# Kernel tuning notes

Measured on AMD Instinct MI355X. Metric: run time of the kernel, lower is better.

## Reference

```python
import jax, jax.numpy as jnp
import numpy as np

WIN = 7
K1, K2 = 0.01, 0.03


def _box_filter(x, w):
    """Valid-padding uniform box filter. x: (B, D, H, W); w: (1, 1, k, k)."""
    B, D, H, Wd = x.shape
    k = w.shape[-1]
    y = jax.lax.conv_general_dilated(
        x.reshape(B * D, 1, H, Wd), w, window_strides=(1, 1), padding='VALID',
        dimension_numbers=('NCHW', 'OIHW', 'NCHW'))
    return y.reshape(B, D, H - k + 1, Wd - k + 1)


def setup_inputs() -> dict:
    key = jax.random.key(0)
    kx, ky = jax.random.split(key)
    X = jax.random.uniform(kx, (4, 64, 256, 256), dtype=jnp.float32)
    Y = jax.random.uniform(ky, (4, 64, 256, 256), dtype=jnp.float32)
    w = jnp.ones((1, 1, WIN, WIN), dtype=jnp.float32) / (WIN * WIN)  # buffer self.w
    return {"X": X, "Y": Y, "w": w}


def reference(X, Y, w):
    data_range = 1.0
    C1 = (K1 * data_range) ** 2
    C2 = (K2 * data_range) ** 2
    NP = WIN * WIN
    cov_norm = NP / (NP - 1)

    ux = _box_filter(X, w)
    uy = _box_filter(Y, w)
    uxx = _box_filter(X * X, w)
    uyy = _box_filter(Y * Y, w)
    uxy = _box_filter(X * Y, w)

    vx = cov_norm * (uxx - ux * ux)
    vy = cov_norm * (uyy - uy * uy)
    vxy = cov_norm * (uxy - ux * uy)

    A1 = 2.0 * ux * uy + C1
    A2 = 2.0 * vxy + C2
    B1 = ux * ux + uy * uy + C1
    B2 = vx + vy + C2
    S = (A1 * A2) / (B1 * B2)  # (B, D, H', W')

    # Faithful to torch: ssim_per_slice[:, i] = S_i.mean() (mean over batch AND spatial),
    # then 1 - mean over depth, returned per batch element.
    slice_means = S.mean(axis=(0, 2, 3))  # (D,)
    loss = 1.0 - slice_means.mean()
    return jnp.full((X.shape[0],), loss, dtype=X.dtype)
```

## Files before the change

### kernel.cpp

```cpp
#include <hip/hip_runtime.h>

#define H 256
#define W 256
#define OWID 250
#define BAND 10
#define NBANDS 25
#define NW 3200
#define WPB 4
#define NBLOCKS (NW / WPB)
#define RIN 16
#define ROWB 1024


__device__ __forceinline__ float4 f4zero() { return make_float4(0.f, 0.f, 0.f, 0.f); }

#define CC1 1e-4f
#define CC2 9e-4f
#define KAA (1.f / 2401.f)
#define K2A (2.f / 2401.f)
#define KT1 (1.f / 24.f)
#define KT2 (-1.f / 1176.f)
#define KT3 (1.f / 48.f)
#define KT4 (-1.f / 2352.f)

struct M4 { float4 sx, sy, sxy, spp; };

__device__ __forceinline__ float4 ld16(const char* b, int off) {
    return *(const float4*)(b + off);
}

__device__ __forceinline__ void slide(M4& m, const float4 xn, const float4 yn,
                                      const float4 xo, const float4 yo) {
    m.sx.x += xn.x - xo.x; m.sx.y += xn.y - xo.y;
    m.sx.z += xn.z - xo.z; m.sx.w += xn.w - xo.w;
    m.sy.x += yn.x - yo.x; m.sy.y += yn.y - yo.y;
    m.sy.z += yn.z - yo.z; m.sy.w += yn.w - yo.w;
    m.sxy.x = fmaf(xn.x, yn.x, fmaf(-xo.x, yo.x, m.sxy.x));
    m.sxy.y = fmaf(xn.y, yn.y, fmaf(-xo.y, yo.y, m.sxy.y));
    m.sxy.z = fmaf(xn.z, yn.z, fmaf(-xo.z, yo.z, m.sxy.z));
    m.sxy.w = fmaf(xn.w, yn.w, fmaf(-xo.w, yo.w, m.sxy.w));
    m.spp.x = fmaf(xn.x, xn.x, fmaf(yn.x, yn.x, fmaf(-xo.x, xo.x, fmaf(-yo.x, yo.x, m.spp.x))));
    m.spp.y = fmaf(xn.y, xn.y, fmaf(yn.y, yn.y, fmaf(-xo.y, xo.y, fmaf(-yo.y, yo.y, m.spp.y))));
    m.spp.z = fmaf(xn.z, xn.z, fmaf(yn.z, yn.z, fmaf(-xo.z, xo.z, fmaf(-yo.z, yo.z, m.spp.z))));
    m.spp.w = fmaf(xn.w, xn.w, fmaf(yn.w, yn.w, fmaf(-xo.w, xo.w, fmaf(-yo.w, yo.w, m.spp.w))));
}

__device__ __forceinline__ void hwin4(const float4 S, float w[4]) {
    const float p1 = S.x;
    const float p2 = p1 + S.y;
    const float p3 = p2 + S.z;
    const float E  = p3 + S.w;
    const float n3 = __shfl_down(p3, 1);
    const float nE = __shfl_down(E, 1);
    const float f1 = __shfl_down(p1, 2);
    const float f2 = __shfl_down(p2, 2);
    w[0] = E + n3;
    w[1] = (E - p1) + nE;
    w[2] = (E - p2) + nE + f1;
    w[3] = (E - p3) + nE + f2;
}

__device__ __forceinline__ void outrow(const M4& m, const float m01,
                                       const float m23, float& lsum) {
    float wx[4], wy[4], wpp[4], wxy[4];
    hwin4(m.sx,  wx);
    hwin4(m.sy,  wy);
    hwin4(m.spp, wpp);
    hwin4(m.sxy, wxy);
    #pragma unroll
    for (int s = 0; s < 4; ++s) {
        const float P  = wx[s] * wy[s];
        const float Qs = fmaf(wy[s], wy[s], wx[s] * wx[s]);
        const float A1 = fmaf(K2A, P, CC1);
        const float B1 = fmaf(KAA, Qs, CC1);
        const float A2 = fmaf(KT1, wxy[s], fmaf(KT2, P, CC2));
        const float B2 = fmaf(KT3, wpp[s], fmaf(KT4, Qs, CC2));
        const float S  = (A1 * A2) * __builtin_amdgcn_rcpf(B1 * B2);
        lsum = fmaf(S, (s < 2) ? m01 : m23, lsum);
    }
}

template<int R>
__device__ __forceinline__ void step(
    const char* XA, const char* YA, const char* XB, const char* YB,
    const int lo, M4& a, M4& b,
    float4& exA, float4& eyA, float4& exB, float4& eyB,
    const float m01, const float m23, float& lsum)
{
    {
        const float4 xn = exA, yn = eyA;
        if constexpr (R + 1 < RIN) {
            exA = ld16(XA, lo + (R + 1) * ROWB);
            eyA = ld16(YA, lo + (R + 1) * ROWB);
        }
        float4 xo = f4zero(), yo = f4zero();
        if constexpr (R >= 7) {
            xo = ld16(XA, lo + (R - 7) * ROWB);
            yo = ld16(YA, lo + (R - 7) * ROWB);
        }
        slide(a, xn, yn, xo, yo);
        if constexpr (R >= 6) outrow(a, m01, m23, lsum);
    }
    {
        const float4 xn = exB, yn = eyB;
        if constexpr (R + 1 < RIN) {
            exB = ld16(XB, lo + (R + 1) * ROWB);
            eyB = ld16(YB, lo + (R + 1) * ROWB);
        }
        float4 xo = f4zero(), yo = f4zero();
        if constexpr (R >= 7) {
            xo = ld16(XB, lo + (R - 7) * ROWB);
            yo = ld16(YB, lo + (R - 7) * ROWB);
        }
        slide(b, xn, yn, xo, yo);
        if constexpr (R >= 6) outrow(b, m01, m23, lsum);
    }
    if constexpr (R + 1 < RIN)
        step<R + 1>(XA, YA, XB, YB, lo, a, b, exA, eyA, exB, eyB, m01, m23, lsum);
}

__global__ __launch_bounds__(256) void ssim_band_kernel(
    const float* __restrict__ X, const float* __restrict__ Y,
    float* __restrict__ partial)
{
    const int lane = threadIdx.x & 63;
    const int wid  = blockIdx.x * WPB + (threadIdx.x >> 6);
    const int imgA = wid / NBANDS;
    const int band = wid % NBANDS;
    const int r0 = band * BAND;

    const size_t baseA = ((size_t)imgA * H + r0) * ROWB;
    const size_t dB    = (size_t)128 * H * ROWB;
    const char* XA = (const char*)X + baseA;
    const char* YA = (const char*)Y + baseA;
    const char* XB = XA + dB;
    const char* YB = YA + dB;
    const int lo = lane * 16;

    M4 a, b;
    a.sx = f4zero(); a.sy = f4zero(); a.sxy = f4zero(); a.spp = f4zero();
    b.sx = f4zero(); b.sy = f4zero(); b.sxy = f4zero(); b.spp = f4zero();

    float4 exA = ld16(XA, lo), eyA = ld16(YA, lo);
    float4 exB = ld16(XB, lo), eyB = ld16(YB, lo);

    const float m01 = (lane <= 62) ? 1.0f : 0.0f;
    const float m23 = (lane <= 61) ? 1.0f : 0.0f;

    float lsum = 0.0f;
    step<0>(XA, YA, XB, YB, lo, a, b, exA, eyA, exB, eyB, m01, m23, lsum);

    #pragma unroll
    for (int off = 32; off > 0; off >>= 1)
        lsum += __shfl_down(lsum, off, 64);
    if (lane == 0) partial[wid] = lsum;
}

__global__ __launch_bounds__(256) void ssim_reduce_kernel(
    const float* __restrict__ partial, float* __restrict__ out)
{
    const int tid = threadIdx.x;
    double acc = 0.0;
    for (int i = tid; i < NW; i += 256)
        acc += (double)partial[i];
    #pragma unroll
    for (int off = 32; off > 0; off >>= 1)
        acc += __shfl_down(acc, off, 64);
    __shared__ double wsumd[4];
    if ((tid & 63) == 0) wsumd[tid >> 6] = acc;
    __syncthreads();
    if (tid == 0) {
        double total = wsumd[0] + wsumd[1] + wsumd[2] + wsumd[3];
        float loss = (float)(1.0 - total / 16000000.0);
        out[0] = loss; out[1] = loss; out[2] = loss; out[3] = loss;
    }
}

extern "C" void kernel_launch(void* const* d_in, const int* in_sizes, int n_in,
                              void* d_out, int out_size, void* d_ws, size_t ws_size,
                              hipStream_t stream) {
    const float* X = (const float*)d_in[0];
    const float* Y = (const float*)d_in[1];
    float* out = (float*)d_out;
    float* partial = (float*)d_ws;

    hipLaunchKernelGGL(ssim_band_kernel, dim3(NBLOCKS), dim3(256), 0, stream,
                       X, Y, partial);
    hipLaunchKernelGGL(ssim_reduce_kernel, dim3(1), dim3(256), 0, stream,
                       partial, out);
}
```

Before: 162.6 us.

## Stage band rows through LDS with async global_load_lds, one image per wave

Replaces direct register loads with global_load_lds (direct global-to-LDS DMA) into a triple-buffered ring for incoming rows and a double-buffered ring for the rows leaving the window, synchronised by explicit vmcnt waits. Each wave now handles one image band instead of two, which doubles the number of waves and partials. The intent is to overlap memory latency with compute and lower register pressure. In exchange it adds LDS traffic, relies on hand-tuned waitcnt counts being correct, and halves the work per wave.

```diff
diff --git a/kernel.cpp b/kernel.cpp
--- a/kernel.cpp
+++ b/kernel.cpp
@@ -2,14 +2,15 @@
 
 #define H 256
 #define W 256
+#define W4 (W / 4)
 #define OWID 250
 #define BAND 10
 #define NBANDS 25
-#define NW 3200
+#define NBLK 6400
+#define RIN 16
 #define WPB 4
-#define NBLOCKS (NW / WPB)
-#define RIN 16
-#define ROWB 1024
+#define NBLOCKS (NBLK / WPB)
+#define SLOTF 512
 
 
 __device__ __forceinline__ float4 f4zero() { return make_float4(0.f, 0.f, 0.f, 0.f); }
@@ -23,11 +24,26 @@
 #define KT3 (1.f / 48.f)
 #define KT4 (-1.f / 2352.f)
 
+__device__ __forceinline__ void stage(const float4* g, float* l) {
+    __builtin_amdgcn_global_load_lds(
+        (const __attribute__((address_space(1))) unsigned int*)g,
+        (__attribute__((address_space(3))) unsigned int*)l,
+        16, 0, 0);
+}
+
+template<int N> __device__ __forceinline__ void wait_vm() {
+    if constexpr (N >= 6)      asm volatile("s_waitcnt vmcnt(6)" ::: "memory");
+    else if constexpr (N == 4) asm volatile("s_waitcnt vmcnt(4)" ::: "memory");
+    else if constexpr (N == 2) asm volatile("s_waitcnt vmcnt(2)" ::: "memory");
+    else                       asm volatile("s_waitcnt vmcnt(0)" ::: "memory");
+    __builtin_amdgcn_sched_barrier(0);
+}
+
+template<int R> constexpr int nwait() {
+    return (R <= 5) ? 4 : (R <= 13) ? 6 : (R == 14) ? 4 : 0;
+}
+
 struct M4 { float4 sx, sy, sxy, spp; };
-
-__device__ __forceinline__ float4 ld16(const char* b, int off) {
-    return *(const float4*)(b + off);
-}
 
 __device__ __forceinline__ void slide(M4& m, const float4 xn, const float4 yn,
                                       const float4 xo, const float4 yo) {
@@ -81,74 +97,68 @@
 }
 
 template<int R>
-__device__ __forceinline__ void step(
-    const char* XA, const char* YA, const char* XB, const char* YB,
-    const int lo, M4& a, M4& b,
-    float4& exA, float4& eyA, float4& exB, float4& eyB,
-    const float m01, const float m23, float& lsum)
+__device__ __forceinline__ void step(const float4* Xp, const float4* Yp,
+                                     float* exl, float* lvl, const int lo4,
+                                     M4& m, const float m01, const float m23,
+                                     float& lsum)
 {
-    {
-        const float4 xn = exA, yn = eyA;
-        if constexpr (R + 1 < RIN) {
-            exA = ld16(XA, lo + (R + 1) * ROWB);
-            eyA = ld16(YA, lo + (R + 1) * ROWB);
-        }
-        float4 xo = f4zero(), yo = f4zero();
-        if constexpr (R >= 7) {
-            xo = ld16(XA, lo + (R - 7) * ROWB);
-            yo = ld16(YA, lo + (R - 7) * ROWB);
-        }
-        slide(a, xn, yn, xo, yo);
-        if constexpr (R >= 6) outrow(a, m01, m23, lsum);
-    }
-    {
-        const float4 xn = exB, yn = eyB;
-        if constexpr (R + 1 < RIN) {
-            exB = ld16(XB, lo + (R + 1) * ROWB);
-            eyB = ld16(YB, lo + (R + 1) * ROWB);
-        }
-        float4 xo = f4zero(), yo = f4zero();
-        if constexpr (R >= 7) {
-            xo = ld16(XB, lo + (R - 7) * ROWB);
-            yo = ld16(YB, lo + (R - 7) * ROWB);
-        }
-        slide(b, xn, yn, xo, yo);
-        if constexpr (R >= 6) outrow(b, m01, m23, lsum);
-    }
+    if constexpr (R >= 6 && R <= 14) {
+        stage(Xp + (R - 6) * W4, lvl + ((R - 6) % 2) * SLOTF);
+        stage(Yp + (R - 6) * W4, lvl + ((R - 6) % 2) * SLOTF + 256);
+    }
+    if constexpr (R + 2 < RIN) {
+        stage(Xp + (R + 2) * W4, exl + ((R + 2) % 3) * SLOTF);
+        stage(Yp + (R + 2) * W4, exl + ((R + 2) % 3) * SLOTF + 256);
+    }
+    wait_vm<nwait<R>()>();
+
+    const float4 xn = *(const float4*)(exl + (R % 3) * SLOTF + lo4);
+    const float4 yn = *(const float4*)(exl + (R % 3) * SLOTF + 256 + lo4);
+    float4 xo = f4zero(), yo = f4zero();
+    if constexpr (R >= 7) {
+        xo = *(const float4*)(lvl + ((R - 7) % 2) * SLOTF + lo4);
+        yo = *(const float4*)(lvl + ((R - 7) % 2) * SLOTF + 256 + lo4);
+    }
+
+    slide(m, xn, yn, xo, yo);
+    if constexpr (R >= 6) outrow(m, m01, m23, lsum);
+
     if constexpr (R + 1 < RIN)
-        step<R + 1>(XA, YA, XB, YB, lo, a, b, exA, eyA, exB, eyB, m01, m23, lsum);
+        step<R + 1>(Xp, Yp, exl, lvl, lo4, m, m01, m23, lsum);
 }
 
 __global__ __launch_bounds__(256) void ssim_band_kernel(
     const float* __restrict__ X, const float* __restrict__ Y,
     float* __restrict__ partial)
 {
-    const int lane = threadIdx.x & 63;
-    const int wid  = blockIdx.x * WPB + (threadIdx.x >> 6);
-    const int imgA = wid / NBANDS;
-    const int band = wid % NBANDS;
+    __shared__ float lds[WPB][5 * SLOTF];
+
+    const int lane  = threadIdx.x & 63;
+    const int wslot = threadIdx.x >> 6;
+    const int wid   = blockIdx.x * WPB + wslot;
+    const int img   = wid / NBANDS;
+    const int band  = wid % NBANDS;
     const int r0 = band * BAND;
 
-    const size_t baseA = ((size_t)imgA * H + r0) * ROWB;
-    const size_t dB    = (size_t)128 * H * ROWB;
-    const char* XA = (const char*)X + baseA;
-    const char* YA = (const char*)Y + baseA;
-    const char* XB = XA + dB;
-    const char* YB = YA + dB;
-    const int lo = lane * 16;
-
-    M4 a, b;
-    a.sx = f4zero(); a.sy = f4zero(); a.sxy = f4zero(); a.spp = f4zero();
-    b.sx = f4zero(); b.sy = f4zero(); b.sxy = f4zero(); b.spp = f4zero();
-
-    float4 exA = ld16(XA, lo), eyA = ld16(YA, lo);
-    float4 exB = ld16(XB, lo), eyB = ld16(YB, lo);
+    const float4* Xp = (const float4*)X + ((size_t)img * H + r0) * W4 + lane;
+    const float4* Yp = (const float4*)Y + ((size_t)img * H + r0) * W4 + lane;
+    float* exl = &lds[wslot][0];
+    float* lvl = &lds[wslot][3 * SLOTF];
+    const int lo4 = lane * 4;
+
+    M4 m;
+    m.sx = f4zero(); m.sy = f4zero(); m.sxy = f4zero(); m.spp = f4zero();
 
     const float m01 = (lane <= 62) ? 1.0f : 0.0f;
     const float m23 = (lane <= 61) ? 1.0f : 0.0f;
 
+    stage(Xp,      exl);
+    stage(Yp,      exl + 256);
+    stage(Xp + W4, exl + SLOTF);
+    stage(Yp + W4, exl + SLOTF + 256);
+
     float lsum = 0.0f;
-    step<0>(XA, YA, XB, YB, lo, a, b, exA, eyA, exB, eyB, m01, m23, lsum);
+    step<0>(Xp, Yp, exl, lvl, lo4, m, m01, m23, lsum);
 
     #pragma unroll
     for (int off = 32; off > 0; off >>= 1)
@@ -161,7 +171,7 @@
 {
     const int tid = threadIdx.x;
     double acc = 0.0;
-    for (int i = tid; i < NW; i += 256)
+    for (int i = tid; i < NBLK; i += 256)
         acc += (double)partial[i];
     #pragma unroll
     for (int off = 32; off > 0; off >>= 1)
```

Result: slower. 172.3 us (+6.0%).
